# Kernel tuning notes

Measured on AMD Instinct MI355X. Metric: run time of the kernel, lower is better.

Reference implementation:

```python
import jax, jax.numpy as jnp
import numpy as np

STAGES = 3
CAUSAL = True


def sine_positional_encoding(T, D, dtype=jnp.float32):
    # keras_nlp SinePositionEncoding: interleaved sin/cos, base 10000
    pos = jnp.arange(T, dtype=dtype)[:, None]            # [T,1]
    i = jnp.arange(D)[None, :]                            # [1,D]
    angle = pos / jnp.power(jnp.asarray(10000.0, dtype), (2 * (i // 2)).astype(dtype) / D)
    return jnp.where(i % 2 == 0, jnp.sin(angle), jnp.cos(angle))  # [T,D]


def setup_inputs() -> dict:
    key = jax.random.key(0)
    kX, kWp, kbp, kWf, kbf = jax.random.split(key, 5)
    B, T, D = 4, 4096, 1024
    X = jax.random.normal(kX, (B, T, D), dtype=jnp.float32)
    # data_projection: D -> (stages+1)*D
    Wp = jax.random.normal(kWp, (D, (STAGES + 1) * D), dtype=jnp.float32) / np.sqrt(D)
    bp = jnp.zeros(((STAGES + 1) * D,), dtype=jnp.float32)
    # filters: D -> stages*D (applied to positional encoding)
    Wf = jax.random.normal(kWf, (D, STAGES * D), dtype=jnp.float32) / np.sqrt(D)
    bf = jnp.zeros((STAGES * D,), dtype=jnp.float32)
    return {"X": X, "Wp": Wp, "bp": bp, "Wf": Wf, "bf": bf}


def reference(X, Wp, bp, Wf, bf):
    B, T, D = X.shape
    # linear projections of data: [B,T,stages+1,D]
    xp = (jnp.einsum('btd,de->bte', X, Wp) + bp).reshape(B, T, STAGES + 1, D)
    # filters from sinusoidal positional encoding (batch-independent): [T,stages,D]
    pos = sine_positional_encoding(T, D, X.dtype)
    f = (pos @ Wf + bf).reshape(T, STAGES, D)
    if CAUSAL:
        # zero-pad time axis to 2T -> circular FFT conv becomes linear (causal) conv
        xp = jnp.concatenate([xp, jnp.zeros_like(xp)], axis=1)   # [B,2T,S+1,D]
        f = jnp.concatenate([f, jnp.zeros_like(f)], axis=0)      # [2T,S,D]
    L = xp.shape[1]
    F = jnp.fft.rfft(f, axis=0)                                   # [L//2+1,S,D]
    y = xp[:, :, 0, :]                                            # [B,L,D]
    for i in range(STAGES):
        conv = jnp.fft.irfft(jnp.fft.rfft(y, axis=1) * F[None, :, i, :], n=L, axis=1)
        y = conv * xp[:, :, i + 1, :]
    return y[:, :T, :] if CAUSAL else y
```

## Files before the change

kernel.cpp:

```cpp
#include <hip/hip_runtime.h>
#include <math.h>

#define T_LEN 4096
#define D_DIM 1024
#define B_DIM 4
#define N_STAGES 3
#define FT 512
#define CT 1024

typedef unsigned short bf16_t;
typedef __bf16 bf16x8 __attribute__((ext_vector_type(8)));
typedef float f32x4 __attribute__((ext_vector_type(4)));

#define PD(i) ((i) + ((((unsigned)(i)) >> 6) << 2))
#define PADN 4352

__device__ __forceinline__ bf16_t f2bf(float f) {
    union { float f; unsigned u; } v; v.f = f;
    unsigned r = v.u + 0x7FFFu + ((v.u >> 16) & 1u);
    return (bf16_t)(r >> 16);
}
__device__ __forceinline__ float bf2f(bf16_t h) {
    union { unsigned u; float f; } v; v.u = ((unsigned)h) << 16;
    return v.f;
}
__device__ __forceinline__ float2 cmul(float2 a, float2 b) {
    return make_float2(a.x * b.x - a.y * b.y, a.x * b.y + a.y * b.x);
}
__device__ __forceinline__ float2 cadd(float2 a, float2 b) { return make_float2(a.x + b.x, a.y + b.y); }
__device__ __forceinline__ float2 csub(float2 a, float2 b) { return make_float2(a.x - b.x, a.y - b.y); }
__device__ __forceinline__ float2 conjf2(float2 a) { return make_float2(a.x, -a.y); }

#define GLOAD_LDS16(gp, lp) __builtin_amdgcn_global_load_lds( \
    (const __attribute__((address_space(1))) void*)(gp),      \
    (__attribute__((address_space(3))) void*)(lp), 16, 0, 0)

__global__ __launch_bounds__(256) void pos_kernel(bf16_t* __restrict__ posbf) {
    int idx = blockIdx.x * 256 + threadIdx.x;
    int t = idx >> 10;
    int k = idx & 1023;
    float e = (float)(k & ~1) / (float)D_DIM;
    float r = exp2f(-e * 13.287712379549449f);
    float angle = (float)t * r;
    float v = (k & 1) ? cosf(angle) : sinf(angle);
    posbf[idx] = f2bf(v);
}

__global__ __launch_bounds__(256) void f32_to_bf16_kernel(const float* __restrict__ in,
                                                          bf16_t* __restrict__ out, int n8) {
    int i = blockIdx.x * 256 + threadIdx.x;
    if (i >= n8) return;
    float4 a = ((const float4*)in)[i * 2];
    float4 b = ((const float4*)in)[i * 2 + 1];
    ((ushort4*)out)[i * 2]     = make_ushort4(f2bf(a.x), f2bf(a.y), f2bf(a.z), f2bf(a.w));
    ((ushort4*)out)[i * 2 + 1] = make_ushort4(f2bf(b.x), f2bf(b.y), f2bf(b.z), f2bf(b.w));
}

__global__ __launch_bounds__(256) void transpose_to_bf16(const float* __restrict__ in,
                                                         bf16_t* __restrict__ out, int K, int N) {
    __shared__ float tile[32][33];
    const int n0 = blockIdx.x * 32;
    const int k0 = blockIdx.y * 32;
    const int tx = threadIdx.x & 31;
    const int ty = threadIdx.x >> 5;
    for (int i = ty; i < 32; i += 8)
        tile[i][tx] = in[(size_t)(k0 + i) * N + n0 + tx];
    __syncthreads();
    for (int i = ty; i < 32; i += 8)
        out[(size_t)(n0 + i) * K + k0 + tx] = f2bf(tile[tx][i]);
}

template <int MODE>
__global__ __launch_bounds__(256) void mfma_gemm(const bf16_t* __restrict__ A,
                                                 const bf16_t* __restrict__ BT,
                                                 const float* __restrict__ bias,
                                                 void* __restrict__ outv,
                                                 int M, int N, int K, int nbx) {
    constexpr int SMEM_BYTES = (MODE == 0) ? (128 * 136 * 2) : (128 * 132 * 4);
    __shared__ __align__(16) char smem[SMEM_BYTES];
    bf16_t* As = (bf16_t*)smem;
    bf16_t* Bs = (bf16_t*)(smem + 8192);

    const int tid = threadIdx.x;
    const int lane = tid & 63;
    const int w = tid >> 6;
    const int wr = w >> 1, wc = w & 1;

    const int nwg = gridDim.x;
    const int q = nwg >> 3;
    const int swz = (blockIdx.x & 7) * q + (blockIdx.x >> 3);
    const int by = swz / nbx, bx = swz - by * nbx;
    const int row0 = by * 128, col0 = bx * 128;

    f32x4 acc[4][4];
#pragma unroll
    for (int m = 0; m < 4; ++m)
#pragma unroll
        for (int n = 0; n < 4; ++n) acc[m][n] = (f32x4)(0.0f);

    int offs[2], rr[2], kk8[2];
#pragma unroll
    for (int c = 0; c < 2; ++c) {
        offs[c] = (w * 2 + c) * 1024 + lane * 16;
        rr[c] = offs[c] >> 6;
        kk8[c] = ((offs[c] >> 4) & 3) * 8;
    }

    for (int k0 = 0; k0 < K; k0 += 32) {
#pragma unroll
        for (int c = 0; c < 2; ++c) {
            const bf16_t* gA = A + (size_t)(row0 + rr[c]) * K + k0 + kk8[c];
            GLOAD_LDS16(gA, As + (w * 2 + c) * 512);
            const bf16_t* gB = BT + (size_t)(col0 + rr[c]) * K + k0 + kk8[c];
            GLOAD_LDS16(gB, Bs + (w * 2 + c) * 512);
        }
        __syncthreads();

        bf16x8 af[4], bfr[4];
#pragma unroll
        for (int m = 0; m < 4; ++m)
            af[m] = *(const bf16x8*)&As[(wr * 64 + m * 16 + (lane & 15)) * 32 + (lane >> 4) * 8];
#pragma unroll
        for (int n = 0; n < 4; ++n)
            bfr[n] = *(const bf16x8*)&Bs[(wc * 64 + n * 16 + (lane & 15)) * 32 + (lane >> 4) * 8];
#pragma unroll
        for (int m = 0; m < 4; ++m)
#pragma unroll
            for (int n = 0; n < 4; ++n)
                acc[m][n] = __builtin_amdgcn_mfma_f32_16x16x32_bf16(af[m], bfr[n], acc[m][n], 0, 0, 0);
        __syncthreads();
    }

    if (MODE == 0) {
        bf16_t* Cs = (bf16_t*)smem;
#pragma unroll
        for (int m = 0; m < 4; ++m)
#pragma unroll
            for (int n = 0; n < 4; ++n) {
                int cl = wc * 64 + n * 16 + (lane & 15);
                int rlb = wr * 64 + m * 16 + ((lane >> 4) << 2);
                float bb = bias[col0 + cl];
#pragma unroll
                for (int j = 0; j < 4; ++j)
                    Cs[cl * 136 + rlb + j] = f2bf(acc[m][n][j] + bb);
            }
        __syncthreads();
        int dl = tid >> 1, th = tid & 1;
        int cc = col0 + dl;
        int s = cc >> 10, d = cc & 1023;
        int b = row0 >> 12;
        int t0 = (row0 & 4095) + th * 64;
        uint4* dst = (uint4*)&((bf16_t*)outv)[((size_t)(s * 4 + b) * 1024 + d) * 4096 + t0];
        const uint4* src = (const uint4*)&Cs[dl * 136 + th * 64];
#pragma unroll
        for (int j = 0; j < 8; ++j) dst[j] = src[j];
    } else {
        float* CsF = (float*)smem;
#pragma unroll
        for (int m = 0; m < 4; ++m)
#pragma unroll
            for (int n = 0; n < 4; ++n) {
                int cl = wc * 64 + n * 16 + (lane & 15);
                int rlb = wr * 64 + m * 16 + ((lane >> 4) << 2);
                float bb = bias[col0 + cl];
#pragma unroll
                for (int j = 0; j < 4; ++j)
                    CsF[cl * 132 + rlb + j] = acc[m][n][j] + bb;
            }
        __syncthreads();
        int dl = tid >> 1, th = tid & 1;
        int cc = col0 + dl;
        uint4* dst = (uint4*)&((float*)outv)[(size_t)cc * 4096 + row0 + th * 64];
        const uint4* src = (const uint4*)&CsF[dl * 132 + th * 64];
#pragma unroll
        for (int j = 0; j < 16; ++j) dst[j] = src[j];
    }
}

template <int INV>
__device__ __forceinline__ void bfly4(float2& a, float2& b, float2& c, float2& d) {
    float2 t0 = cadd(a, c), t1 = csub(a, c), t2 = cadd(b, d), t3 = csub(b, d);
    float2 it3 = INV ? make_float2(-t3.y, t3.x) : make_float2(t3.y, -t3.x);
    a = cadd(t0, t2); b = cadd(t1, it3); c = csub(t0, t2); d = csub(t1, it3);
}

template <int INV>
__device__ __forceinline__ void dft8(float2 (&x)[8]) {
    bfly4<INV>(x[0], x[2], x[4], x[6]);
    bfly4<INV>(x[1], x[3], x[5], x[7]);
    const float s2 = 0.70710678118654752f;
    const float2 o1 = INV ? make_float2(s2, s2) : make_float2(s2, -s2);
    const float2 o3 = INV ? make_float2(-s2, s2) : make_float2(-s2, -s2);
    x[3] = cmul(x[3], o1);
    x[5] = INV ? make_float2(-x[5].y, x[5].x) : make_float2(x[5].y, -x[5].x);
    x[7] = cmul(x[7], o3);
    float2 F0 = cadd(x[0], x[1]), F4 = csub(x[0], x[1]);
    float2 F1 = cadd(x[2], x[3]), F5 = csub(x[2], x[3]);
    float2 F2 = cadd(x[4], x[5]), F6 = csub(x[4], x[5]);
    float2 F3 = cadd(x[6], x[7]), F7 = csub(x[6], x[7]);
    x[0] = F0; x[1] = F1; x[2] = F2; x[3] = F3;
    x[4] = F4; x[5] = F5; x[6] = F6; x[7] = F7;
}

template <int INV, int M>
__device__ __forceinline__ void r8_pass(float2* __restrict__ s, const float2* __restrict__ Wq) {
    const int p = threadIdx.x;
    const int r = p & (M - 1);
    const int jm = p - r;
    float2 x[8];
#pragma unroll
    for (int c = 0; c < 8; ++c) x[c] = s[PD(p + 512 * c)];
    __syncthreads();
    dft8<INV>(x);
    const int base = 8 * jm + r;
    if (M == 512) {
#pragma unroll
        for (int q = 0; q < 8; ++q) s[PD(base + q * 512)] = x[q];
    } else {
        float2 w1 = Wq[jm];
        if (INV) w1.y = -w1.y;
        float2 w2 = cmul(w1, w1);
        float2 w3 = cmul(w2, w1);
        float2 w4 = cmul(w2, w2);
        s[PD(base)]         = x[0];
        s[PD(base + M)]     = cmul(w1, x[1]);
        s[PD(base + 2 * M)] = cmul(w2, x[2]);
        s[PD(base + 3 * M)] = cmul(w3, x[3]);
        s[PD(base + 4 * M)] = cmul(w4, x[4]);
        s[PD(base + 5 * M)] = cmul(cmul(w4, w1), x[5]);
        s[PD(base + 6 * M)] = cmul(cmul(w4, w2), x[6]);
        s[PD(base + 7 * M)] = cmul(cmul(w4, w3), x[7]);
    }
    __syncthreads();
}

template <int INV>
__device__ __forceinline__ void fft4096_ip(float2* __restrict__ s, const float2* __restrict__ Wq) {
    r8_pass<INV, 1>(s, Wq);
    r8_pass<INV, 8>(s, Wq);
    r8_pass<INV, 64>(s, Wq);
    r8_pass<INV, 512>(s, Wq);
}

template <int INV, int M>
__device__ __forceinline__ void r8_pass2(float2 (*__restrict__ s)[PADN],
                                         const float2* __restrict__ Wq) {
    const int p = threadIdx.x & 511;
    const int sb = (threadIdx.x >> 9) << 1;
    const int r = p & (M - 1);
    const int jm = p - r;
    float2 x[2][8];
#pragma unroll
    for (int e = 0; e < 2; ++e)
#pragma unroll
        for (int c = 0; c < 8; ++c) x[e][c] = s[sb + e][PD(p + 512 * c)];
    __syncthreads();
    const int base = 8 * jm + r;
    if (M == 512) {
#pragma unroll
        for (int e = 0; e < 2; ++e) {
            dft8<INV>(x[e]);
#pragma unroll
            for (int q = 0; q < 8; ++q) s[sb + e][PD(base + q * 512)] = x[e][q];
        }
    } else {
        float2 w1 = Wq[jm];
        if (INV) w1.y = -w1.y;
        float2 w2 = cmul(w1, w1);
        float2 w3 = cmul(w2, w1);
        float2 w4 = cmul(w2, w2);
        float2 w5 = cmul(w4, w1);
        float2 w6 = cmul(w4, w2);
        float2 w7 = cmul(w4, w3);
#pragma unroll
        for (int e = 0; e < 2; ++e) {
            dft8<INV>(x[e]);
            s[sb + e][PD(base)]         = x[e][0];
            s[sb + e][PD(base + M)]     = cmul(w1, x[e][1]);
            s[sb + e][PD(base + 2 * M)] = cmul(w2, x[e][2]);
            s[sb + e][PD(base + 3 * M)] = cmul(w3, x[e][3]);
            s[sb + e][PD(base + 4 * M)] = cmul(w4, x[e][4]);
            s[sb + e][PD(base + 5 * M)] = cmul(w5, x[e][5]);
            s[sb + e][PD(base + 6 * M)] = cmul(w6, x[e][6]);
            s[sb + e][PD(base + 7 * M)] = cmul(w7, x[e][7]);
        }
    }
    __syncthreads();
}

template <int INV>
__device__ __forceinline__ void fft4096_ip2(float2 (*__restrict__ s)[PADN],
                                            const float2* __restrict__ Wq) {
    r8_pass2<INV, 1>(s, Wq);
    r8_pass2<INV, 8>(s, Wq);
    r8_pass2<INV, 64>(s, Wq);
    r8_pass2<INV, 512>(s, Wq);
}

template <int NTHR>
__device__ __forceinline__ void init_tables(float2* __restrict__ Wq, float2* __restrict__ Wu) {
    const int tid = threadIdx.x;
    if (NTHR > 512 ? (tid < 512) : true) {
        float sn, cs;
        __sincosf((float)tid * -1.5339807878856412e-3f, &sn, &cs);
        Wq[tid] = make_float2(cs, sn);
    }
#pragma unroll
    for (int u = 0; u < 2048 / NTHR; ++u) {
        int k = u * NTHR + tid;
        float sn, cs;
        __sincosf((float)k * -7.669903939428206e-4f, &sn, &cs);
        Wu[k] = make_float2(cs, sn);
    }
}

__device__ __forceinline__ float2 spec_load(const void* spec, int bf, size_t row, int k) {
    if (bf) {
        ushort2 h = ((const ushort2*)spec)[row * 4097 + k];
        return make_float2(bf2f(h.x), bf2f(h.y));
    }
    return ((const float2*)spec)[row * 4097 + k];
}
__device__ __forceinline__ void spec_store(void* spec, int bf, size_t row, int k, float2 v) {
    if (bf) ((ushort2*)spec)[row * 4097 + k] = make_ushort2(f2bf(v.x), f2bf(v.y));
    else    ((float2*)spec)[row * 4097 + k] = v;
}

__global__ __launch_bounds__(FT)
void filter_fft_kernel(const float* __restrict__ fT,
                       void* __restrict__ specv,
                       int spec_bf16) {
    __shared__ __align__(16) float2 sA[PADN];
    __shared__ float2 Wq[512];
    __shared__ float2 Wu[2048];
    const int tid = threadIdx.x;
    const size_t row = blockIdx.x;
    init_tables<FT>(Wq, Wu);
    const float4* f4 = (const float4*)&fT[row * T_LEN];
#pragma unroll
    for (int u = 0; u < 2; ++u) {
        int j = u * FT + tid;
        float4 v = f4[j];
        sA[PD(2 * j)]     = make_float2(v.x, v.y);
        sA[PD(2 * j + 1)] = make_float2(v.z, v.w);
    }
#pragma unroll
    for (int u = 0; u < 4; ++u) {
        int n = 2048 + u * FT + tid;
        sA[PD(n)] = make_float2(0.0f, 0.0f);
    }
    __syncthreads();
    fft4096_ip<0>(sA, Wq);
#pragma unroll
    for (int u = 0; u < 4; ++u) {
        int s = u * FT + tid;
        if (s < 2047) {
            int k = s + 1, nk = 4096 - k;
            float2 Zk = sA[PD(k)], Zn = sA[PD(nk)];
            float2 Ye = make_float2(0.5f * (Zk.x + Zn.x), 0.5f * (Zk.y - Zn.y));
            float2 Yo = make_float2(0.5f * (Zk.y + Zn.y), -0.5f * (Zk.x - Zn.x));
            float2 w = Wu[k];
            float2 wYo = cmul(w, Yo);
            spec_store(specv, spec_bf16, row, k, cadd(Ye, wYo));
            spec_store(specv, spec_bf16, row, nk, conjf2(csub(Ye, wYo)));
        }
    }
    if (tid == 0) {
        float2 Z0 = sA[PD(0)];
        spec_store(specv, spec_bf16, row, 0,    make_float2(Z0.x + Z0.y, 0.0f));
        spec_store(specv, spec_bf16, row, 4096, make_float2(Z0.x - Z0.y, 0.0f));
        spec_store(specv, spec_bf16, row, 2048, conjf2(sA[PD(2048)]));
    }
}

__global__ __launch_bounds__(CT)
void conv_kernel(const bf16_t* __restrict__ xpT,
                 const void* __restrict__ specv,
                 int spec_bf16,
                 bf16_t* __restrict__ yT) {
    __shared__ __align__(16) float2 sA[4][PADN];
    __shared__ float2 Wq[512];
    __shared__ float2 Wu[2048];
    const int tid = threadIdx.x;
    const int d = blockIdx.x;
    init_tables<CT>(Wq, Wu);

#pragma unroll
    for (int bb = 0; bb < 4; ++bb) {
        const ushort4* y4 = (const ushort4*)&xpT[((size_t)bb * 1024 + d) * T_LEN];
        {
            int j = tid;
            ushort4 h = y4[j];
            sA[bb][PD(2 * j)]     = make_float2(bf2f(h.x), bf2f(h.y));
            sA[bb][PD(2 * j + 1)] = make_float2(bf2f(h.z), bf2f(h.w));
        }
#pragma unroll
        for (int u = 0; u < 2; ++u) {
            int n = 2048 + u * CT + tid;
            sA[bb][PD(n)] = make_float2(0.0f, 0.0f);
        }
    }
    __syncthreads();

    const float scale = 1.0f / 4096.0f;
    for (int st = 0; st < N_STAGES; ++st) {
        fft4096_ip2<0>(sA, Wq);
        const size_t row = (size_t)st * 1024 + d;
#pragma unroll
        for (int u = 0; u < 2; ++u) {
            int s = u * CT + tid;
            if (s < 2047) {
                int k = s + 1, nk = 4096 - k;
                float2 w = Wu[k];
                float2 cw = conjf2(w);
                float2 Fk = spec_load(specv, spec_bf16, row, k);
                float2 Fn = spec_load(specv, spec_bf16, row, nk);
#pragma unroll
                for (int bb = 0; bb < 4; ++bb) {
                    float2 Zk = sA[bb][PD(k)], Zn = sA[bb][PD(nk)];
                    float2 Ye = make_float2(0.5f * (Zk.x + Zn.x), 0.5f * (Zk.y - Zn.y));
                    float2 Yo = make_float2(0.5f * (Zk.y + Zn.y), -0.5f * (Zk.x - Zn.x));
                    float2 wYo = cmul(w, Yo);
                    float2 Yk = cadd(Ye, wYo);
                    float2 Ynk = conjf2(csub(Ye, wYo));
                    float2 Hk = cmul(Yk, Fk);
                    float2 Hn = cmul(Ynk, Fn);
                    float2 He = make_float2(0.5f * (Hk.x + Hn.x), 0.5f * (Hk.y - Hn.y));
                    float2 Hd = make_float2(0.5f * (Hk.x - Hn.x), 0.5f * (Hk.y + Hn.y));
                    float2 Ho = cmul(cw, Hd);
                    sA[bb][PD(k)]  = make_float2(He.x - Ho.y, He.y + Ho.x);
                    sA[bb][PD(nk)] = make_float2(He.x + Ho.y, Ho.x - He.y);
                }
            }
        }
        if (tid == 0) {
            float2 F0 = spec_load(specv, spec_bf16, row, 0);
            float2 FN = spec_load(specv, spec_bf16, row, 4096);
            float2 F2 = spec_load(specv, spec_bf16, row, 2048);
#pragma unroll
            for (int bb = 0; bb < 4; ++bb) {
                float2 Z0 = sA[bb][PD(0)];
                float Y0 = Z0.x + Z0.y, YN = Z0.x - Z0.y;
                float2 H0 = make_float2(Y0 * F0.x, Y0 * F0.y);
                float2 HN = make_float2(YN * FN.x, YN * FN.y);
                float2 He0 = make_float2(0.5f * (H0.x + HN.x), 0.5f * (H0.y + HN.y));
                float2 Ho0 = make_float2(0.5f * (H0.x - HN.x), 0.5f * (H0.y - HN.y));
                sA[bb][PD(0)] = make_float2(He0.x - Ho0.y, He0.y + Ho0.x);
                float2 H2 = cmul(conjf2(sA[bb][PD(2048)]), F2);
                sA[bb][PD(2048)] = conjf2(H2);
            }
        }
        __syncthreads();
        fft4096_ip2<1>(sA, Wq);

        if (st < N_STAGES - 1) {
#pragma unroll
            for (int bb = 0; bb < 4; ++bb) {
                const ushort4* g4 = (const ushort4*)&xpT[((size_t)((st + 1) * 4 + bb) * 1024 + d) * T_LEN];
                {
                    int j = tid;
                    ushort4 h = g4[j];
                    float2 v0 = sA[bb][PD(2 * j)], v1 = sA[bb][PD(2 * j + 1)];
                    sA[bb][PD(2 * j)]     = make_float2(v0.x * scale * bf2f(h.x), v0.y * scale * bf2f(h.y));
                    sA[bb][PD(2 * j + 1)] = make_float2(v1.x * scale * bf2f(h.z), v1.y * scale * bf2f(h.w));
                }
#pragma unroll
                for (int u = 0; u < 2; ++u) {
                    int n = 2048 + u * CT + tid;
                    sA[bb][PD(n)] = make_float2(0.0f, 0.0f);
                }
            }
            __syncthreads();
        } else {
#pragma unroll
            for (int bb = 0; bb < 4; ++bb) {
                const ushort4* g4 = (const ushort4*)&xpT[((size_t)((st + 1) * 4 + bb) * 1024 + d) * T_LEN];
                ushort4* yrow = (ushort4*)&yT[((size_t)bb * 1024 + d) * T_LEN];
                int j = tid;
                ushort4 h = g4[j];
                float2 v0 = sA[bb][PD(2 * j)], v1 = sA[bb][PD(2 * j + 1)];
                yrow[j] = make_ushort4(f2bf(v0.x * scale * bf2f(h.x)),
                                       f2bf(v0.y * scale * bf2f(h.y)),
                                       f2bf(v1.x * scale * bf2f(h.z)),
                                       f2bf(v1.y * scale * bf2f(h.w)));
            }
        }
    }
}

__global__ __launch_bounds__(256) void transpose_out(const bf16_t* __restrict__ yT,
                                                     float* __restrict__ out) {
    __shared__ float tile[32][33];
    const int tb = blockIdx.z;
    const int t0 = blockIdx.x * 32;
    const int d0 = blockIdx.y * 32;
    const int tx = threadIdx.x & 31;
    const int ty = threadIdx.x >> 5;
    for (int i = ty; i < 32; i += 8)
        tile[i][tx] = bf2f(yT[((size_t)tb * 1024 + d0 + i) * 4096 + t0 + tx]);
    __syncthreads();
    for (int i = ty; i < 32; i += 8)
        out[((size_t)tb * 4096 + t0 + i) * 1024 + d0 + tx] = tile[tx][i];
}

extern "C" void kernel_launch(void* const* d_in, const int* in_sizes, int n_in,
                              void* d_out, int out_size, void* d_ws, size_t ws_size,
                              hipStream_t stream) {
    const float* X   = (const float*)d_in[0];
    const float* Wp  = (const float*)d_in[1];
    const float* bp  = (const float*)d_in[2];
    const float* Wf  = (const float*)d_in[3];
    const float* bfv = (const float*)d_in[4];
    float* out = (float*)d_out;
    char* ws = (char*)d_ws;

    const size_t XPT_BYTES  = (size_t)134217728;
    const size_t SPEC_F32_B = (size_t)3 * 1024 * 4097 * 8;
    const size_t SPEC_BF_B  = (size_t)3 * 1024 * 4097 * 4;
    const size_t XBF_BYTES  = (size_t)33554432;
    const size_t WPT_BYTES  = (size_t)8388608;

    bf16_t* xpT   = (bf16_t*)ws;
    bf16_t* posbf = (bf16_t*)ws;
    bf16_t* WfT   = (bf16_t*)(ws + 16777216);
    float*  fT    = (float*)(ws + 33554432);
    void*   spec  = (void*)(ws + XPT_BYTES);

    int spec_bf16;
    size_t spec_bytes;
    if (ws_size >= XPT_BYTES + SPEC_F32_B + XBF_BYTES + WPT_BYTES) {
        spec_bf16 = 0; spec_bytes = SPEC_F32_B;
    } else {
        spec_bf16 = 1; spec_bytes = SPEC_BF_B;
    }
    bf16_t* Xbf = (bf16_t*)(ws + XPT_BYTES + spec_bytes);
    bf16_t* WpT = (bf16_t*)(ws + XPT_BYTES + spec_bytes + XBF_BYTES);
    bf16_t* yT  = Xbf;

    pos_kernel<<<(T_LEN * D_DIM) / 256, 256, 0, stream>>>(posbf);

    transpose_to_bf16<<<dim3(3072 / 32, 1024 / 32), 256, 0, stream>>>(Wf, WfT, 1024, 3072);
    mfma_gemm<1><<<768, 256, 0, stream>>>(posbf, WfT, bfv, fT, 4096, 3072, 1024, 24);

    filter_fft_kernel<<<N_STAGES * D_DIM, FT, 0, stream>>>(fT, spec, spec_bf16);

    f32_to_bf16_kernel<<<8192, 256, 0, stream>>>(X, Xbf, 2097152);
    transpose_to_bf16<<<dim3(4096 / 32, 1024 / 32), 256, 0, stream>>>(Wp, WpT, 1024, 4096);
    mfma_gemm<0><<<4096, 256, 0, stream>>>(Xbf, WpT, bp, xpT, 16384, 4096, 1024, 32);

    conv_kernel<<<D_DIM, CT, 0, stream>>>(xpT, spec, spec_bf16, yT);

    transpose_out<<<dim3(4096 / 32, 1024 / 32, B_DIM), 256, 0, stream>>>(yT, out);
}
```

Before: 691.3 us.

## Process FFT batches sequentially per thread, change LDS padding, drop Wq table

The radix-8 FFT pass now has each thread handle one signal at a time: it works on one signal half, syncs, then works on the other, instead of holding two signals' worth of values in registers at once. This lowers register pressure, but each pass now needs twice as many barriers. The LDS padding changes from 4 entries per 64 to 1 per 8 to alter the bank-conflict pattern, which grows the shared-memory footprint. The separate Wq twiddle table is removed and its values are read as every other entry of Wu.

```diff
diff --git a/kernel.cpp b/kernel.cpp
--- a/kernel.cpp
+++ b/kernel.cpp
@@ -12,8 +12,8 @@
 typedef __bf16 bf16x8 __attribute__((ext_vector_type(8)));
 typedef float f32x4 __attribute__((ext_vector_type(4)));
 
-#define PD(i) ((i) + ((((unsigned)(i)) >> 6) << 2))
-#define PADN 4352
+#define PD(i) ((i) + (((unsigned)(i)) >> 3))
+#define PADN 4607
 
 __device__ __forceinline__ bf16_t f2bf(float f) {
     union { float f; unsigned u; } v; v.f = f;
@@ -203,7 +203,7 @@
 }
 
 template <int INV, int M>
-__device__ __forceinline__ void r8_pass(float2* __restrict__ s, const float2* __restrict__ Wq) {
+__device__ __forceinline__ void r8_pass(float2* __restrict__ s, const float2* __restrict__ Wu) {
     const int p = threadIdx.x;
     const int r = p & (M - 1);
     const int jm = p - r;
@@ -217,7 +217,7 @@
 #pragma unroll
         for (int q = 0; q < 8; ++q) s[PD(base + q * 512)] = x[q];
     } else {
-        float2 w1 = Wq[jm];
+        float2 w1 = Wu[2 * jm];
         if (INV) w1.y = -w1.y;
         float2 w2 = cmul(w1, w1);
         float2 w3 = cmul(w2, w1);
@@ -235,76 +235,79 @@
 }
 
 template <int INV>
-__device__ __forceinline__ void fft4096_ip(float2* __restrict__ s, const float2* __restrict__ Wq) {
-    r8_pass<INV, 1>(s, Wq);
-    r8_pass<INV, 8>(s, Wq);
-    r8_pass<INV, 64>(s, Wq);
-    r8_pass<INV, 512>(s, Wq);
+__device__ __forceinline__ void fft4096_ip(float2* __restrict__ s, const float2* __restrict__ Wu) {
+    r8_pass<INV, 1>(s, Wu);
+    r8_pass<INV, 8>(s, Wu);
+    r8_pass<INV, 64>(s, Wu);
+    r8_pass<INV, 512>(s, Wu);
 }
 
 template <int INV, int M>
-__device__ __forceinline__ void r8_pass2(float2 (*__restrict__ s)[PADN],
-                                         const float2* __restrict__ Wq) {
+__device__ __forceinline__ void r8_pass4x(float2 (*__restrict__ s)[PADN],
+                                          const float2* __restrict__ Wu) {
     const int p = threadIdx.x & 511;
-    const int sb = (threadIdx.x >> 9) << 1;
+    const int half = threadIdx.x >> 9;
     const int r = p & (M - 1);
     const int jm = p - r;
-    float2 x[2][8];
-#pragma unroll
-    for (int e = 0; e < 2; ++e)
-#pragma unroll
-        for (int c = 0; c < 8; ++c) x[e][c] = s[sb + e][PD(p + 512 * c)];
-    __syncthreads();
     const int base = 8 * jm + r;
+    float2 w1, w2, w3, w4, w5, w6, w7;
+    if (M != 512) {
+        w1 = Wu[2 * jm];
+        if (INV) w1.y = -w1.y;
+        w2 = cmul(w1, w1); w3 = cmul(w2, w1); w4 = cmul(w2, w2);
+        w5 = cmul(w4, w1); w6 = cmul(w4, w2); w7 = cmul(w4, w3);
+    }
+    float2 x[8];
+#pragma unroll
+    for (int c = 0; c < 8; ++c) x[c] = s[half][PD(p + 512 * c)];
+    __syncthreads();
+    dft8<INV>(x);
     if (M == 512) {
 #pragma unroll
-        for (int e = 0; e < 2; ++e) {
-            dft8<INV>(x[e]);
-#pragma unroll
-            for (int q = 0; q < 8; ++q) s[sb + e][PD(base + q * 512)] = x[e][q];
-        }
+        for (int q = 0; q < 8; ++q) s[half][PD(base + q * 512)] = x[q];
     } else {
-        float2 w1 = Wq[jm];
-        if (INV) w1.y = -w1.y;
-        float2 w2 = cmul(w1, w1);
-        float2 w3 = cmul(w2, w1);
-        float2 w4 = cmul(w2, w2);
-        float2 w5 = cmul(w4, w1);
-        float2 w6 = cmul(w4, w2);
-        float2 w7 = cmul(w4, w3);
-#pragma unroll
-        for (int e = 0; e < 2; ++e) {
-            dft8<INV>(x[e]);
-            s[sb + e][PD(base)]         = x[e][0];
-            s[sb + e][PD(base + M)]     = cmul(w1, x[e][1]);
-            s[sb + e][PD(base + 2 * M)] = cmul(w2, x[e][2]);
-            s[sb + e][PD(base + 3 * M)] = cmul(w3, x[e][3]);
-            s[sb + e][PD(base + 4 * M)] = cmul(w4, x[e][4]);
-            s[sb + e][PD(base + 5 * M)] = cmul(w5, x[e][5]);
-            s[sb + e][PD(base + 6 * M)] = cmul(w6, x[e][6]);
-            s[sb + e][PD(base + 7 * M)] = cmul(w7, x[e][7]);
-        }
+        s[half][PD(base)]         = x[0];
+        s[half][PD(base + M)]     = cmul(w1, x[1]);
+        s[half][PD(base + 2 * M)] = cmul(w2, x[2]);
+        s[half][PD(base + 3 * M)] = cmul(w3, x[3]);
+        s[half][PD(base + 4 * M)] = cmul(w4, x[4]);
+        s[half][PD(base + 5 * M)] = cmul(w5, x[5]);
+        s[half][PD(base + 6 * M)] = cmul(w6, x[6]);
+        s[half][PD(base + 7 * M)] = cmul(w7, x[7]);
+    }
+    float2 y[8];
+#pragma unroll
+    for (int c = 0; c < 8; ++c) y[c] = s[2 + half][PD(p + 512 * c)];
+    __syncthreads();
+    dft8<INV>(y);
+    if (M == 512) {
+#pragma unroll
+        for (int q = 0; q < 8; ++q) s[2 + half][PD(base + q * 512)] = y[q];
+    } else {
+        s[2 + half][PD(base)]         = y[0];
+        s[2 + half][PD(base + M)]     = cmul(w1, y[1]);
+        s[2 + half][PD(base + 2 * M)] = cmul(w2, y[2]);
+        s[2 + half][PD(base + 3 * M)] = cmul(w3, y[3]);
+        s[2 + half][PD(base + 4 * M)] = cmul(w4, y[4]);
+        s[2 + half][PD(base + 5 * M)] = cmul(w5, y[5]);
+        s[2 + half][PD(base + 6 * M)] = cmul(w6, y[6]);
+        s[2 + half][PD(base + 7 * M)] = cmul(w7, y[7]);
     }
     __syncthreads();
 }
 
 template <int INV>
-__device__ __forceinline__ void fft4096_ip2(float2 (*__restrict__ s)[PADN],
-                                            const float2* __restrict__ Wq) {
-    r8_pass2<INV, 1>(s, Wq);
-    r8_pass2<INV, 8>(s, Wq);
-    r8_pass2<INV, 64>(s, Wq);
-    r8_pass2<INV, 512>(s, Wq);
+__device__ __forceinline__ void fft4096_ip4x(float2 (*__restrict__ s)[PADN],
+                                             const float2* __restrict__ Wu) {
+    r8_pass4x<INV, 1>(s, Wu);
+    r8_pass4x<INV, 8>(s, Wu);
+    r8_pass4x<INV, 64>(s, Wu);
+    r8_pass4x<INV, 512>(s, Wu);
 }
 
 template <int NTHR>
-__device__ __forceinline__ void init_tables(float2* __restrict__ Wq, float2* __restrict__ Wu) {
+__device__ __forceinline__ void init_wu(float2* __restrict__ Wu) {
     const int tid = threadIdx.x;
-    if (NTHR > 512 ? (tid < 512) : true) {
-        float sn, cs;
-        __sincosf((float)tid * -1.5339807878856412e-3f, &sn, &cs);
-        Wq[tid] = make_float2(cs, sn);
-    }
 #pragma unroll
     for (int u = 0; u < 2048 / NTHR; ++u) {
         int k = u * NTHR + tid;
@@ -331,11 +334,10 @@
                        void* __restrict__ specv,
                        int spec_bf16) {
     __shared__ __align__(16) float2 sA[PADN];
-    __shared__ float2 Wq[512];
-    __shared__ float2 Wu[2048];
+    __shared__ __align__(16) float2 Wu[2048];
     const int tid = threadIdx.x;
     const size_t row = blockIdx.x;
-    init_tables<FT>(Wq, Wu);
+    init_wu<FT>(Wu);
     const float4* f4 = (const float4*)&fT[row * T_LEN];
 #pragma unroll
     for (int u = 0; u < 2; ++u) {
@@ -350,7 +352,7 @@
         sA[PD(n)] = make_float2(0.0f, 0.0f);
     }
     __syncthreads();
-    fft4096_ip<0>(sA, Wq);
+    fft4096_ip<0>(sA, Wu);
 #pragma unroll
     for (int u = 0; u < 4; ++u) {
         int s = u * FT + tid;
@@ -379,11 +381,10 @@
                  int spec_bf16,
                  bf16_t* __restrict__ yT) {
     __shared__ __align__(16) float2 sA[4][PADN];
-    __shared__ float2 Wq[512];
-    __shared__ float2 Wu[2048];
+    __shared__ __align__(16) float2 Wu[2048];
     const int tid = threadIdx.x;
     const int d = blockIdx.x;
-    init_tables<CT>(Wq, Wu);
+    init_wu<CT>(Wu);
 
 #pragma unroll
     for (int bb = 0; bb < 4; ++bb) {
@@ -404,7 +405,7 @@
 
     const float scale = 1.0f / 4096.0f;
     for (int st = 0; st < N_STAGES; ++st) {
-        fft4096_ip2<0>(sA, Wq);
+        fft4096_ip4x<0>(sA, Wu);
         const size_t row = (size_t)st * 1024 + d;
 #pragma unroll
         for (int u = 0; u < 2; ++u) {
@@ -451,7 +452,7 @@
             }
         }
         __syncthreads();
-        fft4096_ip2<1>(sA, Wq);
+        fft4096_ip4x<1>(sA, Wu);
 
         if (st < N_STAGES - 1) {
 #pragma unroll
```

New measurement: 721.8 us. 1.04x slower.
